# Kernel optimization log

Measured on AMD Instinct MI355X. Metric: run time of the kernel, lower is better.

The kernel has to match this reference:

```python
import jax, jax.numpy as jnp
import numpy as np

IN_F, ASS, OUT_F = 1024, 100000, 1024
P = 0.0005
NUM_ROUNDS = 24  # fixed replacement for the data-dependent convergence loop
TOTAL = IN_F + ASS + OUT_F


def _build_graph(seed=0):
    """Random digraph: input->assoc and assoc->(assoc|out) with prob P,
    plus guaranteed edges so the propagation_check of the original passes
    (every assoc node reachable, every output has an in-edge)."""
    rng = np.random.default_rng(seed)
    ass0, out0 = IN_F, IN_F + ASS
    n_ie = int(P * IN_F * ASS)
    ie_src = rng.integers(0, IN_F, n_ie)
    ie_dst = rng.integers(ass0, out0, n_ie)
    n_ae = int(P * ASS * (ASS + OUT_F))
    ae_src = rng.integers(ass0, out0, n_ae)
    ae_dst = rng.integers(ass0, out0 + OUT_F, n_ae)
    # guarantee reachability: assoc node j gets an in-edge from a random node < j
    g_dst = np.arange(ass0, out0)
    g_src = (rng.random(ASS) * g_dst).astype(np.int64)
    gi = g_src < IN_F
    ie_src = np.concatenate([ie_src, g_src[gi]])
    ie_dst = np.concatenate([ie_dst, g_dst[gi]])
    ae_src = np.concatenate([ae_src, g_src[~gi]])
    ae_dst = np.concatenate([ae_dst, g_dst[~gi]])
    # every output neuron gets at least one in-edge from a random assoc
    ae_src = np.concatenate([ae_src, rng.integers(ass0, out0, OUT_F)])
    ae_dst = np.concatenate([ae_dst, np.arange(out0, out0 + OUT_F)])
    return ie_src, ie_dst, ae_src, ae_dst


def setup_inputs() -> dict:
    key = jax.random.key(0)
    k1, k2, k3 = jax.random.split(key, 3)
    ie_src, ie_dst, ae_src, ae_dst = _build_graph()
    x = jax.random.normal(k1, (1, IN_F), jnp.float32)
    # nn.init.uniform_(w, -1, 1)
    input_weights = jax.random.uniform(k2, (len(ie_src),), jnp.float32, -1.0, 1.0)
    assoc_weights = jax.random.uniform(k3, (len(ae_src),), jnp.float32, -1.0, 1.0)
    return {
        'x': x,
        'input_weights': input_weights,
        'assoc_weights': assoc_weights,
        'in_edge_src': jnp.asarray(ie_src, jnp.int32),
        'in_edge_dst': jnp.asarray(ie_dst, jnp.int32),
        'ass_edge_src': jnp.asarray(ae_src, jnp.int32),
        'ass_edge_dst': jnp.asarray(ae_dst, jnp.int32),
    }


def _forward(x, input_weights, assoc_weights, in_edge_src, in_edge_dst,
             ass_edge_src, ass_edge_dst):
    idx = jnp.arange(TOTAL)
    is_assoc = (idx >= IN_F) & (idx < IN_F + ASS)
    # --- input phase: each input neuron i sends x[i]*w along its out-edges ---
    msgs = x[0][in_edge_src] * input_weights              # [E_in]
    mem = jax.ops.segment_sum(msgs, in_edge_dst, num_segments=TOTAL)
    recv = jax.ops.segment_sum(jnp.ones_like(in_edge_dst), in_edge_dst,
                               num_segments=TOTAL) > 0
    status = jnp.where(recv, 1, 0).astype(jnp.int32)      # 0=inactive,1=working,2=activated

    # --- synchronous wave propagation through associative neurons ---
    def step(carry, _):
        mem, status = carry
        fire = (status == 1) & is_assoc                    # working assoc neurons fire
        src_fire = fire[ass_edge_src]
        # forward_fn(memory, w) = activation(sum(memory)) * w  (tanh activation)
        vals = jnp.where(src_fire, jnp.tanh(mem[ass_edge_src]) * assoc_weights, 0.0)
        delta = jax.ops.segment_sum(vals, ass_edge_dst, num_segments=TOTAL)
        got = jax.ops.segment_sum(src_fire.astype(jnp.int32), ass_edge_dst,
                                  num_segments=TOTAL) > 0
        mem = jnp.where(fire, 0.0, mem) + delta            # fired neurons erase memory
        status = jnp.where(fire, 2, jnp.where(got & (status == 0), 1, status))
        return (mem, status), None

    (mem, status), _ = jax.lax.scan(step, (mem, status), None, length=NUM_ROUNDS)
    # --- output phase: Y[i] = activation(sum(memory)) * 1 ---
    return jnp.tanh(mem[IN_F + ASS:])


def reference(x, input_weights, assoc_weights, in_edge_src, in_edge_dst,
              ass_edge_src, ass_edge_dst):
    return _forward(x, input_weights, assoc_weights, in_edge_src, in_edge_dst,
                    ass_edge_src, ass_edge_dst)
```

## Files before the change

kernel.cpp:

```cpp
#include <hip/hip_runtime.h>
#include <hip/hip_cooperative_groups.h>

namespace cg = cooperative_groups;

#define IN_F 1024
#define ASS 100000
#define OUT_F 1024
#define TOTAL (IN_F + ASS + OUT_F)
#define ASS0 IN_F
#define OUT0 (IN_F + ASS)
#define NDST (ASS + OUT_F)
#define NUM_ROUNDS 24

#define BIN_SZ 512
#define BIN_SH 9
#define BIN_MK 511
#define NBINS ((NDST + BIN_SZ - 1) / BIN_SZ)
#define NCON 512
#define CON_T 1024
#define SPLIT 8
#define NBM32 3136
#define A0FLAG 0x80000000u

typedef int i4v __attribute__((ext_vector_type(4)));
typedef float f4v __attribute__((ext_vector_type(4)));
typedef unsigned int u2v __attribute__((ext_vector_type(2)));


__global__ __launch_bounds__(256) void kz(float* mem, u2v* ltv, int* flags,
                                          int* bin_cursor, int* scur,
                                          unsigned* bm, int cap, int scap) {
  int i = blockIdx.x * 256 + threadIdx.x;
  int gs = gridDim.x * 256;
  u2v init;
  init.x = 255u;
  init.y = 0u;
  for (int k = i; k < TOTAL; k += gs) {
    mem[k] = 0.f;
    ltv[k] = init;
  }
  for (int k = i; k < NBINS; k += gs) {
    bin_cursor[k] = k * cap;
    scur[k] = k * scap;
  }
  for (int k = i; k < NBM32; k += gs) bm[k] = 0u;
  if (i < 32) flags[i] = 0;
}

__global__ __launch_bounds__(256) void ki(const float* __restrict__ x,
                                          const float* __restrict__ iw,
                                          const int* __restrict__ ies,
                                          const int* __restrict__ ied, int E_in,
                                          float* mem, unsigned int* ltv_raw,
                                          unsigned* bm) {
  int e = blockIdx.x * 256 + threadIdx.x;
  if (e < E_in) {
    int d = ied[e];
    atomicAdd(&mem[d], x[ies[e]] * iw[e]);
    ltv_raw[2 * d] = 0u;
    int b = d - ASS0;
    atomicOr(&bm[b >> 5], 1u << (b & 31));
  }
}

__global__ __launch_bounds__(CON_T) void kc(const int* __restrict__ aes,
                                            const int* __restrict__ aed,
                                            const float* __restrict__ aw,
                                            int E_a, int* bin_cursor,
                                            const unsigned* __restrict__ bm,
                                            u2v* __restrict__ csr, float* mem,
                                            u2v* ltv) {
  for (int i = blockIdx.x * CON_T + (int)threadIdx.x; i < ASS;
       i += NCON * CON_T) {
    int node = ASS0 + i;
    u2v lt = ltv[node];
    if (lt.x == 0u) {
      lt.y = __float_as_uint(tanhf(mem[node]));
      ltv[node] = lt;
      mem[node] = 0.f;
    }
  }
  __shared__ unsigned sbm[NBM32];
  __shared__ int h[4][NBINS];
  __shared__ int cur[NBINS];
  for (int k = threadIdx.x; k < NBM32; k += CON_T) sbm[k] = bm[k];
  for (int b = threadIdx.x; b < 4 * NBINS; b += CON_T)
    h[b / NBINS][b % NBINS] = 0;
  __syncthreads();
  int cp = (threadIdx.x >> 6) & 3;
  const i4v* aed4 = (const i4v*)aed;
  const i4v* aes4 = (const i4v*)aes;
  const f4v* aw4 = (const f4v*)aw;
  int nv4 = E_a >> 2;
  int chunk4 = (nv4 + NCON - 1) / NCON;
  int v0 = blockIdx.x * chunk4;
  int v1 = min(v0 + chunk4, nv4);
  int bv = v0 + (int)threadIdx.x;

  i4v dreg0, dreg1, dreg2;
#pragma unroll
  for (int k = 0; k < 3; ++k) {
    int v = bv + k * CON_T;
    if (v < v1) {
      i4v d4 = aed4[v];
      if (k == 0) dreg0 = d4;
      if (k == 1) dreg1 = d4;
      if (k == 2) dreg2 = d4;
      atomicAdd(&h[cp][(d4.x - ASS0) >> BIN_SH], 1);
      atomicAdd(&h[cp][(d4.y - ASS0) >> BIN_SH], 1);
      atomicAdd(&h[cp][(d4.z - ASS0) >> BIN_SH], 1);
      atomicAdd(&h[cp][(d4.w - ASS0) >> BIN_SH], 1);
    }
  }
  for (int v = bv + 3 * CON_T; v < v1; v += CON_T) {
    i4v d4 = aed4[v];
    atomicAdd(&h[cp][(d4.x - ASS0) >> BIN_SH], 1);
    atomicAdd(&h[cp][(d4.y - ASS0) >> BIN_SH], 1);
    atomicAdd(&h[cp][(d4.z - ASS0) >> BIN_SH], 1);
    atomicAdd(&h[cp][(d4.w - ASS0) >> BIN_SH], 1);
  }
  if (blockIdx.x == 0) {
    for (int e = (nv4 << 2) + (int)threadIdx.x; e < E_a; e += CON_T)
      atomicAdd(&h[cp][(aed[e] - ASS0) >> BIN_SH], 1);
  }
  __syncthreads();
  for (int b = threadIdx.x; b < NBINS; b += CON_T) {
    int c = h[0][b] + h[1][b] + h[2][b] + h[3][b];
    cur[b] = c ? atomicAdd(&bin_cursor[b], c) : 0;
  }
  __syncthreads();
#pragma unroll
  for (int k = 0; k < 3; ++k) {
    int v = bv + k * CON_T;
    if (v < v1) {
      i4v d4 = (k == 0) ? dreg0 : (k == 1) ? dreg1 : dreg2;
      i4v s4 = __builtin_nontemporal_load(&aes4[v]);
      f4v w4 = __builtin_nontemporal_load(&aw4[v]);
#pragma unroll
      for (int j = 0; j < 4; ++j) {
        int d = d4[j] - ASS0;
        int si = s4[j] - ASS0;
        unsigned fl = ((sbm[si >> 5] >> (si & 31)) & 1u) ? A0FLAG : 0u;
        int pos = atomicAdd(&cur[d >> BIN_SH], 1);
        u2v q;
        q.x = fl | ((unsigned)s4[j] << BIN_SH) | (unsigned)(d & BIN_MK);
        q.y = __float_as_uint(w4[j]);
        csr[pos] = q;
      }
    }
  }
  for (int v = bv + 3 * CON_T; v < v1; v += CON_T) {
    i4v d4 = aed4[v];
    i4v s4 = __builtin_nontemporal_load(&aes4[v]);
    f4v w4 = __builtin_nontemporal_load(&aw4[v]);
#pragma unroll
    for (int j = 0; j < 4; ++j) {
      int d = d4[j] - ASS0;
      int si = s4[j] - ASS0;
      unsigned fl = ((sbm[si >> 5] >> (si & 31)) & 1u) ? A0FLAG : 0u;
      int pos = atomicAdd(&cur[d >> BIN_SH], 1);
      u2v q;
      q.x = fl | ((unsigned)s4[j] << BIN_SH) | (unsigned)(d & BIN_MK);
      q.y = __float_as_uint(w4[j]);
      csr[pos] = q;
    }
  }
  if (blockIdx.x == 0) {
    for (int e = (nv4 << 2) + (int)threadIdx.x; e < E_a; e += CON_T) {
      int d = aed[e] - ASS0;
      int si = aes[e] - ASS0;
      unsigned fl = ((sbm[si >> 5] >> (si & 31)) & 1u) ? A0FLAG : 0u;
      int pos = atomicAdd(&cur[d >> BIN_SH], 1);
      u2v q;
      q.x = fl | ((unsigned)aes[e] << BIN_SH) | (unsigned)(d & BIN_MK);
      q.y = __float_as_uint(aw[e]);
      csr[pos] = q;
    }
  }
}

__global__ __launch_bounds__(256) void kRe(int r, int collect, int* flags,
                                           const int* __restrict__ bin_cursor,
                                           const u2v* __restrict__ csr,
                                           const u2v* __restrict__ ltv,
                                           float* __restrict__ gslice,
                                           char* __restrict__ gmask,
                                           u2v* __restrict__ ssur, int* scur,
                                           int cap, int scap) {
  if (r > 0 && flags[r] == 0) return;
  __shared__ float slice[BIN_SZ];
  __shared__ int smask[BIN_SZ];
  int tid = threadIdx.x;
  for (int i = tid; i < BIN_SZ; i += 256) {
    slice[i] = 0.f;
    smask[i] = 0;
  }
  __syncthreads();
  int bin = blockIdx.x >> 3;
  int sub = blockIdx.x & (SPLIT - 1);
  int e0 = bin * cap;
  int e1 = bin_cursor[bin];
  int len = e1 - e0;
  int chunk = (len + SPLIT - 1) / SPLIT;
  int s0 = e0 + sub * chunk;
  int s1 = min(s0 + chunk, e1);
  unsigned rl = (unsigned)r;
#pragma unroll 4
  for (int e = s0 + tid; e < s1; e += 256) {
    u2v q = __builtin_nontemporal_load(&csr[e]);
    if (r == 0) {
      if (q.x & A0FLAG) {
        u2v lt = ltv[(q.x & ~A0FLAG) >> BIN_SH];
        atomicAdd(&slice[q.x & BIN_MK],
                  __uint_as_float(lt.y) * __uint_as_float(q.y));
        smask[q.x & BIN_MK] = 1;
      }
    } else if (!(q.x & A0FLAG)) {
      u2v lt = ltv[q.x >> BIN_SH];
      if (lt.x == rl) {
        atomicAdd(&slice[q.x & BIN_MK],
                  __uint_as_float(lt.y) * __uint_as_float(q.y));
        smask[q.x & BIN_MK] = 1;
      } else if (collect && lt.x == 255u) {
        int pos = atomicAdd(&scur[bin], 1);
        if (pos < bin * scap + scap)
          ssur[pos] = q;
        else
          flags[30] = 1;
      }
    }
  }
  __syncthreads();
  int base = blockIdx.x * BIN_SZ;
  for (int i = tid; i < BIN_SZ; i += 256) {
    gslice[base + i] = slice[i];
    gmask[base + i] = (char)smask[i];
  }
}

__device__ __forceinline__ void mergeEpi(int r, int bin, int stride,
                                         const float* __restrict__ gslice,
                                         const char* __restrict__ gmask,
                                         float* __restrict__ mem,
                                         u2v* __restrict__ ltv, int* flags) {
  for (int t = threadIdx.x; t < BIN_SZ; t += stride) {
    float sv = 0.f;
    int mk = 0;
    int base = bin * SPLIT * BIN_SZ + t;
#pragma unroll
    for (int s = 0; s < SPLIT; ++s) {
      sv += gslice[base + s * BIN_SZ];
      mk |= (int)gmask[base + s * BIN_SZ];
    }
    int d = bin * BIN_SZ + t;
    if (d < NDST && mk) {
      int node = ASS0 + d;
      float nv = mem[node] + sv;
      u2v lt = ltv[node];
      if (lt.x == 255u) {
        u2v nl;
        nl.x = (unsigned)(r + 1);
        if (node < OUT0) {
          nl.y = __float_as_uint(tanhf(nv));
          ltv[node] = nl;
          mem[node] = 0.f;
          flags[r + 1] = 1;
        } else {
          nl.y = 0u;
          ltv[node] = nl;
          mem[node] = nv;
        }
      } else {
        mem[node] = nv;
      }
    }
  }
}

__global__ __launch_bounds__(512) void kRn(int r, int* flags,
                                           const float* __restrict__ gslice,
                                           const char* __restrict__ gmask,
                                           float* __restrict__ mem,
                                           u2v* __restrict__ ltv) {
  if (r > 0 && flags[r] == 0) return;
  mergeEpi(r, blockIdx.x, 512, gslice, gmask, mem, ltv, flags);
}

__global__ __launch_bounds__(1024) void kTail(
    int* flags, const int* __restrict__ bin_cursor,
    const u2v* __restrict__ csr, const u2v* __restrict__ ssur,
    const int* __restrict__ scur, float* __restrict__ mem,
    u2v* __restrict__ ltv, const float* __restrict__ gslice,
    const char* __restrict__ gmask, float* __restrict__ out, int cap,
    int scap) {
  cg::grid_group g = cg::this_grid();
  __shared__ float slice[BIN_SZ];
  __shared__ int smask[BIN_SZ];
  int tid = threadIdx.x;
  int bin = blockIdx.x;
  if (flags[1] != 0) mergeEpi(1, bin, 1024, gslice, gmask, mem, ltv, flags);
  g.sync();
  bool useS = (flags[30] == 0);
  int e0 = useS ? bin * scap : bin * cap;
  int e1 = useS ? min(scur[bin], bin * scap + scap) : bin_cursor[bin];
  const u2v* E = useS ? ssur : csr;
  for (int r = 2; r < NUM_ROUNDS; ++r) {
    if (flags[r] == 0) break;
    if (tid < BIN_SZ) {
      slice[tid] = 0.f;
      smask[tid] = 0;
    }
    __syncthreads();
    unsigned rl = (unsigned)r;
    for (int e = e0 + tid; e < e1; e += 1024) {
      u2v q = E[e];
      u2v lt = ltv[(q.x & ~A0FLAG) >> BIN_SH];
      if (lt.x == rl) {
        atomicAdd(&slice[q.x & BIN_MK],
                  __uint_as_float(lt.y) * __uint_as_float(q.y));
        smask[q.x & BIN_MK] = 1;
      }
    }
    __syncthreads();
    if (tid < BIN_SZ) {
      int d = bin * BIN_SZ + tid;
      if (d < NDST && smask[tid]) {
        int node = ASS0 + d;
        float nv = mem[node] + slice[tid];
        u2v lt = ltv[node];
        if (lt.x == 255u) {
          u2v nl;
          nl.x = (unsigned)(r + 1);
          if (node < OUT0) {
            nl.y = __float_as_uint(tanhf(nv));
            ltv[node] = nl;
            mem[node] = 0.f;
            flags[r + 1] = 1;
          } else {
            nl.y = 0u;
            ltv[node] = nl;
            mem[node] = nv;
          }
        } else {
          mem[node] = nv;
        }
      }
    }
    __syncthreads();
    g.sync();
  }
  if (tid < BIN_SZ) {
    int d = bin * BIN_SZ + tid;
    int node = ASS0 + d;
    if (d < NDST && node >= OUT0) out[node - OUT0] = tanhf(mem[node]);
  }
}


__global__ __launch_bounds__(256) void ko(const float* __restrict__ mem,
                                          float* __restrict__ out) {
  int i = blockIdx.x * 256 + threadIdx.x;
  if (i < OUT_F) out[i] = tanhf(mem[OUT0 + i]);
}
__global__ __launch_bounds__(256) void k_init(float* mem, float* delta,
                                              int* status, int* got) {
  int i = blockIdx.x * 256 + threadIdx.x;
  if (i < TOTAL) {
    mem[i] = 0.f;
    delta[i] = 0.f;
    status[i] = 0;
    got[i] = 0;
  }
}
__global__ __launch_bounds__(256) void k_input(const float* __restrict__ x,
                                               const float* __restrict__ w,
                                               const int* __restrict__ src,
                                               const int* __restrict__ dst,
                                               int n, float* mem, int* got) {
  for (int e = blockIdx.x * 256 + threadIdx.x; e < n; e += gridDim.x * 256) {
    atomicAdd(&mem[dst[e]], x[src[e]] * w[e]);
    got[dst[e]] = 1;
  }
}
__global__ __launch_bounds__(256) void k_status0(int* status, int* got) {
  int i = blockIdx.x * 256 + threadIdx.x;
  if (i < TOTAL) {
    status[i] = got[i] ? 1 : 0;
    got[i] = 0;
  }
}
__global__ __launch_bounds__(256) void k_edge(const float* __restrict__ w,
                                              const int* __restrict__ src,
                                              const int* __restrict__ dst,
                                              int n,
                                              const float* __restrict__ mem,
                                              const int* __restrict__ status,
                                              float* delta, int* got) {
  for (int e = blockIdx.x * 256 + threadIdx.x; e < n; e += gridDim.x * 256) {
    int s = src[e];
    if (status[s] == 1) {
      atomicAdd(&delta[dst[e]], tanhf(mem[s]) * w[e]);
      got[dst[e]] = 1;
    }
  }
}
__global__ __launch_bounds__(256) void k_update(float* mem, float* delta,
                                                int* status, int* got) {
  int i = blockIdx.x * 256 + threadIdx.x;
  if (i < TOTAL) {
    int st = status[i];
    bool fire = (st == 1) && (i >= ASS0) && (i < OUT0);
    float d = delta[i];
    mem[i] = fire ? d : (mem[i] + d);
    status[i] = fire ? 2 : ((got[i] && st == 0) ? 1 : st);
    delta[i] = 0.f;
    got[i] = 0;
  }
}

extern "C" void kernel_launch(void* const* d_in, const int* in_sizes, int n_in,
                              void* d_out, int out_size, void* d_ws,
                              size_t ws_size, hipStream_t stream) {
  const float* x = (const float*)d_in[0];
  const float* iw = (const float*)d_in[1];
  const float* aw = (const float*)d_in[2];
  const int* ies = (const int*)d_in[3];
  const int* ied = (const int*)d_in[4];
  const int* aes = (const int*)d_in[5];
  const int* aed = (const int*)d_in[6];
  int E_in = in_sizes[1];
  int E_a = in_sizes[2];
  float* out = (float*)d_out;
  char* ws = (char*)d_ws;

  int cap = (((E_a / NBINS) * 13) / 10 + 255) & ~255;
  int scap = cap / 4;

  size_t off_csr = 0;
  size_t off_ssur = off_csr + (size_t)NBINS * cap * 8;
  size_t off_ltv = off_ssur + (size_t)NBINS * scap * 8;
  size_t off_mem = off_ltv + (size_t)TOTAL * 8;
  size_t off_bcur = off_mem + (size_t)TOTAL * 4;
  size_t off_scur = off_bcur + (size_t)NBINS * 4;
  size_t off_flags = off_scur + (size_t)NBINS * 4;
  size_t off_bm = off_flags + 32 * 4;
  size_t off_gsl = off_bm + (size_t)NBM32 * 4;
  size_t off_gmk = off_gsl + (size_t)NBINS * SPLIT * BIN_SZ * 4;
  size_t need = off_gmk + (size_t)NBINS * SPLIT * BIN_SZ;

  if (ws_size >= need) {
    u2v* csr = (u2v*)(ws + off_csr);
    u2v* ssur = (u2v*)(ws + off_ssur);
    u2v* ltv = (u2v*)(ws + off_ltv);
    float* mem = (float*)(ws + off_mem);
    int* bin_cursor = (int*)(ws + off_bcur);
    int* scur = (int*)(ws + off_scur);
    int* flags = (int*)(ws + off_flags);
    unsigned* bm = (unsigned*)(ws + off_bm);
    float* gslice = (float*)(ws + off_gsl);
    char* gmask = ws + off_gmk;

    kz<<<(TOTAL + 255) / 256, 256, 0, stream>>>(mem, ltv, flags, bin_cursor,
                                                scur, bm, cap, scap);
    ki<<<(E_in + 255) / 256, 256, 0, stream>>>(x, iw, ies, ied, E_in, mem,
                                               (unsigned int*)ltv, bm);
    kc<<<NCON, CON_T, 0, stream>>>(aes, aed, aw, E_a, bin_cursor, bm, csr,
                                   mem, ltv);

    for (int r = 0; r < 2; ++r) {
      kRe<<<NBINS * SPLIT, 256, 0, stream>>>(r, r == 1 ? 1 : 0, flags,
                                             bin_cursor, csr, ltv, gslice,
                                             gmask, ssur, scur, cap, scap);
      if (r == 0)
        kRn<<<NBINS, 512, 0, stream>>>(r, flags, gslice, gmask, mem, ltv);
    }
    void* targs[] = {(void*)&flags,  (void*)&bin_cursor, (void*)&csr,
                     (void*)&ssur,   (void*)&scur,       (void*)&mem,
                     (void*)&ltv,    (void*)&gslice,     (void*)&gmask,
                     (void*)&out,    (void*)&cap,        (void*)&scap};
    hipLaunchCooperativeKernel((void*)kTail, dim3(NBINS), dim3(1024), targs, 0,
                               stream);
    return;
  }

  float* mem = (float*)ws;
  float* delta = mem + TOTAL;
  int* status = (int*)(delta + TOTAL);
  int* got = status + TOTAL;
  const int nodeBlocks = (TOTAL + 255) / 256;
  k_init<<<nodeBlocks, 256, 0, stream>>>(mem, delta, status, got);
  int inBlocks = (E_in + 255) / 256;
  if (inBlocks > 1024) inBlocks = 1024;
  k_input<<<inBlocks, 256, 0, stream>>>(x, iw, ies, ied, E_in, mem, got);
  k_status0<<<nodeBlocks, 256, 0, stream>>>(status, got);
  int eBlocks = (E_a + 255) / 256;
  if (eBlocks > 2048) eBlocks = 2048;
  for (int r = 0; r < NUM_ROUNDS; ++r) {
    k_edge<<<eBlocks, 256, 0, stream>>>(aw, aes, aed, E_a, mem, status, delta,
                                        got);
    k_update<<<nodeBlocks, 256, 0, stream>>>(mem, delta, status, got);
  }
  ko<<<(OUT_F + 255) / 256, 256, 0, stream>>>(mem, out);
}
```

Measured before the change: 158.3 us.

## Partition each CSR bin into round-0 and later-round segments from both ends

Each destination bin's edge list is now split into two regions: edges whose source fires in round 0 are packed from the bin start, and all other edges are packed from the bin end using a decrementing cursor. Round 0 then scans only its own segment, and later rounds and the tail kernel scan only the remainder, instead of reading every edge and filtering on a flag bit. Bin size also doubles to 1024 destinations, with merge blocks widened to match. The cost is a second histogram and cursor set in the construction kernel and an extra bitmap lookup per edge in the counting pass.

```diff
diff --git a/kernel.cpp b/kernel.cpp
--- a/kernel.cpp
+++ b/kernel.cpp
@@ -12,15 +12,14 @@
 #define NDST (ASS + OUT_F)
 #define NUM_ROUNDS 24
 
-#define BIN_SZ 512
-#define BIN_SH 9
-#define BIN_MK 511
+#define BIN_SZ 1024
+#define BIN_SH 10
+#define BIN_MK 1023
 #define NBINS ((NDST + BIN_SZ - 1) / BIN_SZ)
 #define NCON 512
 #define CON_T 1024
 #define SPLIT 8
 #define NBM32 3136
-#define A0FLAG 0x80000000u
 
 typedef int i4v __attribute__((ext_vector_type(4)));
 typedef float f4v __attribute__((ext_vector_type(4)));
@@ -28,7 +27,7 @@
 
 
 __global__ __launch_bounds__(256) void kz(float* mem, u2v* ltv, int* flags,
-                                          int* bin_cursor, int* scur,
+                                          int* binA, int* binR, int* scur,
                                           unsigned* bm, int cap, int scap) {
   int i = blockIdx.x * 256 + threadIdx.x;
   int gs = gridDim.x * 256;
@@ -40,7 +39,8 @@
     ltv[k] = init;
   }
   for (int k = i; k < NBINS; k += gs) {
-    bin_cursor[k] = k * cap;
+    binA[k] = k * cap;
+    binR[k] = (k + 1) * cap;
     scur[k] = k * scap;
   }
   for (int k = i; k < NBM32; k += gs) bm[k] = 0u;
@@ -66,7 +66,7 @@
 __global__ __launch_bounds__(CON_T) void kc(const int* __restrict__ aes,
                                             const int* __restrict__ aed,
                                             const float* __restrict__ aw,
-                                            int E_a, int* bin_cursor,
+                                            int E_a, int* binA, int* binR,
                                             const unsigned* __restrict__ bm,
                                             u2v* __restrict__ csr, float* mem,
                                             u2v* ltv) {
@@ -81,13 +81,17 @@
     }
   }
   __shared__ unsigned sbm[NBM32];
-  __shared__ int h[4][NBINS];
-  __shared__ int cur[NBINS];
+  __shared__ int hA[2][NBINS], hR[2][NBINS];
+  __shared__ int cA[NBINS], cR[NBINS];
   for (int k = threadIdx.x; k < NBM32; k += CON_T) sbm[k] = bm[k];
-  for (int b = threadIdx.x; b < 4 * NBINS; b += CON_T)
-    h[b / NBINS][b % NBINS] = 0;
+  for (int b = threadIdx.x; b < NBINS; b += CON_T) {
+    hA[0][b] = 0;
+    hA[1][b] = 0;
+    hR[0][b] = 0;
+    hR[1][b] = 0;
+  }
   __syncthreads();
-  int cp = (threadIdx.x >> 6) & 3;
+  int cp = (threadIdx.x >> 6) & 1;
   const i4v* aed4 = (const i4v*)aed;
   const i4v* aes4 = (const i4v*)aes;
   const f4v* aw4 = (const f4v*)aw;
@@ -97,53 +101,68 @@
   int v1 = min(v0 + chunk4, nv4);
   int bv = v0 + (int)threadIdx.x;
 
-  i4v dreg0, dreg1, dreg2;
+  i4v dr0, dr1, dr2, sr0, sr1, sr2;
 #pragma unroll
   for (int k = 0; k < 3; ++k) {
     int v = bv + k * CON_T;
     if (v < v1) {
       i4v d4 = aed4[v];
-      if (k == 0) dreg0 = d4;
-      if (k == 1) dreg1 = d4;
-      if (k == 2) dreg2 = d4;
-      atomicAdd(&h[cp][(d4.x - ASS0) >> BIN_SH], 1);
-      atomicAdd(&h[cp][(d4.y - ASS0) >> BIN_SH], 1);
-      atomicAdd(&h[cp][(d4.z - ASS0) >> BIN_SH], 1);
-      atomicAdd(&h[cp][(d4.w - ASS0) >> BIN_SH], 1);
+      i4v s4 = aes4[v];
+      if (k == 0) { dr0 = d4; sr0 = s4; }
+      if (k == 1) { dr1 = d4; sr1 = s4; }
+      if (k == 2) { dr2 = d4; sr2 = s4; }
+#pragma unroll
+      for (int j = 0; j < 4; ++j) {
+        int b = (d4[j] - ASS0) >> BIN_SH;
+        int si = s4[j] - ASS0;
+        bool a0 = (sbm[si >> 5] >> (si & 31)) & 1u;
+        atomicAdd(a0 ? &hA[cp][b] : &hR[cp][b], 1);
+      }
     }
   }
   for (int v = bv + 3 * CON_T; v < v1; v += CON_T) {
     i4v d4 = aed4[v];
-    atomicAdd(&h[cp][(d4.x - ASS0) >> BIN_SH], 1);
-    atomicAdd(&h[cp][(d4.y - ASS0) >> BIN_SH], 1);
-    atomicAdd(&h[cp][(d4.z - ASS0) >> BIN_SH], 1);
-    atomicAdd(&h[cp][(d4.w - ASS0) >> BIN_SH], 1);
+    i4v s4 = aes4[v];
+#pragma unroll
+    for (int j = 0; j < 4; ++j) {
+      int b = (d4[j] - ASS0) >> BIN_SH;
+      int si = s4[j] - ASS0;
+      bool a0 = (sbm[si >> 5] >> (si & 31)) & 1u;
+      atomicAdd(a0 ? &hA[cp][b] : &hR[cp][b], 1);
+    }
   }
   if (blockIdx.x == 0) {
-    for (int e = (nv4 << 2) + (int)threadIdx.x; e < E_a; e += CON_T)
-      atomicAdd(&h[cp][(aed[e] - ASS0) >> BIN_SH], 1);
+    for (int e = (nv4 << 2) + (int)threadIdx.x; e < E_a; e += CON_T) {
+      int b = (aed[e] - ASS0) >> BIN_SH;
+      int si = aes[e] - ASS0;
+      bool a0 = (sbm[si >> 5] >> (si & 31)) & 1u;
+      atomicAdd(a0 ? &hA[cp][b] : &hR[cp][b], 1);
+    }
   }
   __syncthreads();
   for (int b = threadIdx.x; b < NBINS; b += CON_T) {
-    int c = h[0][b] + h[1][b] + h[2][b] + h[3][b];
-    cur[b] = c ? atomicAdd(&bin_cursor[b], c) : 0;
+    int ca = hA[0][b] + hA[1][b];
+    int cr = hR[0][b] + hR[1][b];
+    cA[b] = ca ? atomicAdd(&binA[b], ca) : 0;
+    cR[b] = cr ? (atomicSub(&binR[b], cr) - cr) : 0;
   }
   __syncthreads();
 #pragma unroll
   for (int k = 0; k < 3; ++k) {
     int v = bv + k * CON_T;
     if (v < v1) {
-      i4v d4 = (k == 0) ? dreg0 : (k == 1) ? dreg1 : dreg2;
-      i4v s4 = __builtin_nontemporal_load(&aes4[v]);
+      i4v d4 = (k == 0) ? dr0 : (k == 1) ? dr1 : dr2;
+      i4v s4 = (k == 0) ? sr0 : (k == 1) ? sr1 : sr2;
       f4v w4 = __builtin_nontemporal_load(&aw4[v]);
 #pragma unroll
       for (int j = 0; j < 4; ++j) {
         int d = d4[j] - ASS0;
+        int b = d >> BIN_SH;
         int si = s4[j] - ASS0;
-        unsigned fl = ((sbm[si >> 5] >> (si & 31)) & 1u) ? A0FLAG : 0u;
-        int pos = atomicAdd(&cur[d >> BIN_SH], 1);
+        bool a0 = (sbm[si >> 5] >> (si & 31)) & 1u;
+        int pos = atomicAdd(a0 ? &cA[b] : &cR[b], 1);
         u2v q;
-        q.x = fl | ((unsigned)s4[j] << BIN_SH) | (unsigned)(d & BIN_MK);
+        q.x = ((unsigned)s4[j] << BIN_SH) | (unsigned)(d & BIN_MK);
         q.y = __float_as_uint(w4[j]);
         csr[pos] = q;
       }
@@ -151,16 +170,17 @@
   }
   for (int v = bv + 3 * CON_T; v < v1; v += CON_T) {
     i4v d4 = aed4[v];
-    i4v s4 = __builtin_nontemporal_load(&aes4[v]);
+    i4v s4 = aes4[v];
     f4v w4 = __builtin_nontemporal_load(&aw4[v]);
 #pragma unroll
     for (int j = 0; j < 4; ++j) {
       int d = d4[j] - ASS0;
+      int b = d >> BIN_SH;
       int si = s4[j] - ASS0;
-      unsigned fl = ((sbm[si >> 5] >> (si & 31)) & 1u) ? A0FLAG : 0u;
-      int pos = atomicAdd(&cur[d >> BIN_SH], 1);
+      bool a0 = (sbm[si >> 5] >> (si & 31)) & 1u;
+      int pos = atomicAdd(a0 ? &cA[b] : &cR[b], 1);
       u2v q;
-      q.x = fl | ((unsigned)s4[j] << BIN_SH) | (unsigned)(d & BIN_MK);
+      q.x = ((unsigned)s4[j] << BIN_SH) | (unsigned)(d & BIN_MK);
       q.y = __float_as_uint(w4[j]);
       csr[pos] = q;
     }
@@ -168,19 +188,21 @@
   if (blockIdx.x == 0) {
     for (int e = (nv4 << 2) + (int)threadIdx.x; e < E_a; e += CON_T) {
       int d = aed[e] - ASS0;
+      int b = d >> BIN_SH;
       int si = aes[e] - ASS0;
-      unsigned fl = ((sbm[si >> 5] >> (si & 31)) & 1u) ? A0FLAG : 0u;
-      int pos = atomicAdd(&cur[d >> BIN_SH], 1);
+      bool a0 = (sbm[si >> 5] >> (si & 31)) & 1u;
+      int pos = atomicAdd(a0 ? &cA[b] : &cR[b], 1);
       u2v q;
-      q.x = fl | ((unsigned)aes[e] << BIN_SH) | (unsigned)(d & BIN_MK);
+      q.x = ((unsigned)aes[e] << BIN_SH) | (unsigned)(d & BIN_MK);
       q.y = __float_as_uint(aw[e]);
       csr[pos] = q;
     }
   }
 }
 
-__global__ __launch_bounds__(256) void kRe(int r, int collect, int* flags,
-                                           const int* __restrict__ bin_cursor,
+__global__ __launch_bounds__(256) void kRe(int r, int* flags,
+                                           const int* __restrict__ binA,
+                                           const int* __restrict__ binR,
                                            const u2v* __restrict__ csr,
                                            const u2v* __restrict__ ltv,
                                            float* __restrict__ gslice,
@@ -198,30 +220,27 @@
   __syncthreads();
   int bin = blockIdx.x >> 3;
   int sub = blockIdx.x & (SPLIT - 1);
-  int e0 = bin * cap;
-  int e1 = bin_cursor[bin];
+  int e0 = (r == 0) ? bin * cap : binR[bin];
+  int e1 = (r == 0) ? binA[bin] : (bin + 1) * cap;
   int len = e1 - e0;
   int chunk = (len + SPLIT - 1) / SPLIT;
   int s0 = e0 + sub * chunk;
   int s1 = min(s0 + chunk, e1);
-  unsigned rl = (unsigned)r;
 #pragma unroll 4
   for (int e = s0 + tid; e < s1; e += 256) {
     u2v q = __builtin_nontemporal_load(&csr[e]);
     if (r == 0) {
-      if (q.x & A0FLAG) {
-        u2v lt = ltv[(q.x & ~A0FLAG) >> BIN_SH];
+      u2v lt = ltv[q.x >> BIN_SH];
+      atomicAdd(&slice[q.x & BIN_MK],
+                __uint_as_float(lt.y) * __uint_as_float(q.y));
+      smask[q.x & BIN_MK] = 1;
+    } else {
+      u2v lt = ltv[q.x >> BIN_SH];
+      if (lt.x == 1u) {
         atomicAdd(&slice[q.x & BIN_MK],
                   __uint_as_float(lt.y) * __uint_as_float(q.y));
         smask[q.x & BIN_MK] = 1;
-      }
-    } else if (!(q.x & A0FLAG)) {
-      u2v lt = ltv[q.x >> BIN_SH];
-      if (lt.x == rl) {
-        atomicAdd(&slice[q.x & BIN_MK],
-                  __uint_as_float(lt.y) * __uint_as_float(q.y));
-        smask[q.x & BIN_MK] = 1;
-      } else if (collect && lt.x == 255u) {
+      } else if (lt.x == 255u) {
         int pos = atomicAdd(&scur[bin], 1);
         if (pos < bin * scap + scap)
           ssur[pos] = q;
@@ -277,22 +296,21 @@
   }
 }
 
-__global__ __launch_bounds__(512) void kRn(int r, int* flags,
-                                           const float* __restrict__ gslice,
-                                           const char* __restrict__ gmask,
-                                           float* __restrict__ mem,
-                                           u2v* __restrict__ ltv) {
+__global__ __launch_bounds__(1024) void kRn(int r, int* flags,
+                                            const float* __restrict__ gslice,
+                                            const char* __restrict__ gmask,
+                                            float* __restrict__ mem,
+                                            u2v* __restrict__ ltv) {
   if (r > 0 && flags[r] == 0) return;
-  mergeEpi(r, blockIdx.x, 512, gslice, gmask, mem, ltv, flags);
+  mergeEpi(r, blockIdx.x, 1024, gslice, gmask, mem, ltv, flags);
 }
 
 __global__ __launch_bounds__(1024) void kTail(
-    int* flags, const int* __restrict__ bin_cursor,
-    const u2v* __restrict__ csr, const u2v* __restrict__ ssur,
-    const int* __restrict__ scur, float* __restrict__ mem,
-    u2v* __restrict__ ltv, const float* __restrict__ gslice,
-    const char* __restrict__ gmask, float* __restrict__ out, int cap,
-    int scap) {
+    int* flags, const int* __restrict__ binR, const u2v* __restrict__ csr,
+    const u2v* __restrict__ ssur, const int* __restrict__ scur,
+    float* __restrict__ mem, u2v* __restrict__ ltv,
+    const float* __restrict__ gslice, const char* __restrict__ gmask,
+    float* __restrict__ out, int cap, int scap) {
   cg::grid_group g = cg::this_grid();
   __shared__ float slice[BIN_SZ];
   __shared__ int smask[BIN_SZ];
@@ -301,8 +319,8 @@
   if (flags[1] != 0) mergeEpi(1, bin, 1024, gslice, gmask, mem, ltv, flags);
   g.sync();
   bool useS = (flags[30] == 0);
-  int e0 = useS ? bin * scap : bin * cap;
-  int e1 = useS ? min(scur[bin], bin * scap + scap) : bin_cursor[bin];
+  int e0 = useS ? bin * scap : binR[bin];
+  int e1 = useS ? min(scur[bin], bin * scap + scap) : (bin + 1) * cap;
   const u2v* E = useS ? ssur : csr;
   for (int r = 2; r < NUM_ROUNDS; ++r) {
     if (flags[r] == 0) break;
@@ -314,7 +332,7 @@
     unsigned rl = (unsigned)r;
     for (int e = e0 + tid; e < e1; e += 1024) {
       u2v q = E[e];
-      u2v lt = ltv[(q.x & ~A0FLAG) >> BIN_SH];
+      u2v lt = ltv[q.x >> BIN_SH];
       if (lt.x == rl) {
         atomicAdd(&slice[q.x & BIN_MK],
                   __uint_as_float(lt.y) * __uint_as_float(q.y));
@@ -440,8 +458,9 @@
   size_t off_ssur = off_csr + (size_t)NBINS * cap * 8;
   size_t off_ltv = off_ssur + (size_t)NBINS * scap * 8;
   size_t off_mem = off_ltv + (size_t)TOTAL * 8;
-  size_t off_bcur = off_mem + (size_t)TOTAL * 4;
-  size_t off_scur = off_bcur + (size_t)NBINS * 4;
+  size_t off_bA = off_mem + (size_t)TOTAL * 4;
+  size_t off_bR = off_bA + (size_t)NBINS * 4;
+  size_t off_scur = off_bR + (size_t)NBINS * 4;
   size_t off_flags = off_scur + (size_t)NBINS * 4;
   size_t off_bm = off_flags + 32 * 4;
   size_t off_gsl = off_bm + (size_t)NBM32 * 4;
@@ -453,31 +472,32 @@
     u2v* ssur = (u2v*)(ws + off_ssur);
     u2v* ltv = (u2v*)(ws + off_ltv);
     float* mem = (float*)(ws + off_mem);
-    int* bin_cursor = (int*)(ws + off_bcur);
+    int* binA = (int*)(ws + off_bA);
+    int* binR = (int*)(ws + off_bR);
     int* scur = (int*)(ws + off_scur);
     int* flags = (int*)(ws + off_flags);
     unsigned* bm = (unsigned*)(ws + off_bm);
     float* gslice = (float*)(ws + off_gsl);
     char* gmask = ws + off_gmk;
 
-    kz<<<(TOTAL + 255) / 256, 256, 0, stream>>>(mem, ltv, flags, bin_cursor,
+    kz<<<(TOTAL + 255) / 256, 256, 0, stream>>>(mem, ltv, flags, binA, binR,
                                                 scur, bm, cap, scap);
     ki<<<(E_in + 255) / 256, 256, 0, stream>>>(x, iw, ies, ied, E_in, mem,
                                                (unsigned int*)ltv, bm);
-    kc<<<NCON, CON_T, 0, stream>>>(aes, aed, aw, E_a, bin_cursor, bm, csr,
+    kc<<<NCON, CON_T, 0, stream>>>(aes, aed, aw, E_a, binA, binR, bm, csr,
                                    mem, ltv);
 
     for (int r = 0; r < 2; ++r) {
-      kRe<<<NBINS * SPLIT, 256, 0, stream>>>(r, r == 1 ? 1 : 0, flags,
-                                             bin_cursor, csr, ltv, gslice,
-                                             gmask, ssur, scur, cap, scap);
+      kRe<<<NBINS * SPLIT, 256, 0, stream>>>(r, flags, binA, binR, csr, ltv,
+                                             gslice, gmask, ssur, scur, cap,
+                                             scap);
       if (r == 0)
-        kRn<<<NBINS, 512, 0, stream>>>(r, flags, gslice, gmask, mem, ltv);
-    }
-    void* targs[] = {(void*)&flags,  (void*)&bin_cursor, (void*)&csr,
-                     (void*)&ssur,   (void*)&scur,       (void*)&mem,
-                     (void*)&ltv,    (void*)&gslice,     (void*)&gmask,
-                     (void*)&out,    (void*)&cap,        (void*)&scap};
+        kRn<<<NBINS, 1024, 0, stream>>>(r, flags, gslice, gmask, mem, ltv);
+    }
+    void* targs[] = {(void*)&flags, (void*)&binR,   (void*)&csr,
+                     (void*)&ssur,  (void*)&scur,   (void*)&mem,
+                     (void*)&ltv,   (void*)&gslice, (void*)&gmask,
+                     (void*)&out,   (void*)&cap,    (void*)&scap};
     hipLaunchCooperativeKernel((void*)kTail, dim3(NBINS), dim3(1024), targs, 0,
                                stream);
     return;
```

After: 157.4 us. No clear change (-0.6%).
